# Optimization experiments

Measured on AMD Instinct MI355X. Metric: run time of the kernel, lower is better.

The kernel has to match this reference:

```python
import jax, jax.numpy as jnp
import numpy as np

C = 1024
MID = C // 4  # 256
B, H, W = 16, 56, 56


def setup_inputs() -> dict:
    key = jax.random.key(0)
    ks = jax.random.split(key, 8)
    x = jax.random.normal(ks[0], (B, C, H, W), dtype=jnp.float32)
    gate_values = jax.random.uniform(ks[1], (B, MID), dtype=jnp.float32)
    # MoELayer conv weights: stack of out_channels 1x1 convs -> [out, in]
    W1 = jax.random.normal(ks[2], (MID, C), dtype=jnp.float32) * (1.0 / np.sqrt(C))
    b1 = jnp.zeros((MID,), dtype=jnp.float32)
    W2 = jax.random.normal(ks[3], (MID, MID), dtype=jnp.float32) * (1.0 / np.sqrt(MID))
    b2 = jnp.zeros((MID,), dtype=jnp.float32)
    W3 = jax.random.normal(ks[4], (C, MID), dtype=jnp.float32) * (1.0 / np.sqrt(MID))
    b3 = jnp.zeros((C,), dtype=jnp.float32)
    return {"x": x, "gate_values": gate_values, "W1": W1, "b1": b1,
            "W2": W2, "b2": b2, "W3": W3, "b3": b3}


def _moe_1x1(h, gate, Wc, bc):
    # Dense equivalent of the per-channel gated 1x1 conv experts:
    # out[b,o] = (conv_o(h[b]) ) * gate[b,o] if gate[b,o] > 0 else 0
    y = jnp.einsum('bchw,oc->bohw', h, Wc) + bc[None, :, None, None]
    g = jnp.where(gate > 0, gate, 0.0)  # [B, O]
    return y * g[:, :, None, None]


def reference(x, gate_values, W1, b1, W2, b2, W3, b3):
    h = jax.nn.relu(_moe_1x1(x, gate_values, W1, b1))
    h = jax.nn.relu(_moe_1x1(h, gate_values, W2, b2))
    h = jax.nn.relu(jnp.einsum('bchw,oc->bohw', h, W3) + b3[None, :, None, None])
    return h + x
```

## Files before the change

### kernel.cpp

```cpp
#include <hip/hip_runtime.h>


#define NPIX 3136
#define BATCH 16

typedef __attribute__((ext_vector_type(8))) short short8;
typedef __attribute__((ext_vector_type(4))) float v4f;

__device__ __forceinline__ unsigned short f2bf(float f) {
    union { float f; unsigned u; } v; v.f = f;
    unsigned r = v.u + 0x7fffu + ((v.u >> 16) & 1u);
    return (unsigned short)(r >> 16);
}

__device__ __forceinline__ void ld_g2l16(const unsigned short* g, unsigned short* l) {
    __builtin_amdgcn_global_load_lds(
        (const __attribute__((address_space(1))) unsigned int*)g,
        (__attribute__((address_space(3))) unsigned int*)l,
        16, 0, 0);
}

__device__ __forceinline__ void stage_w(const unsigned short* wg, int rowstride,
                                        unsigned short* wr, int t) {
    ld_g2l16(wg,                  wr + t * 8);
    ld_g2l16(wg + 64 * rowstride, wr + 2048 + t * 8);
    ld_g2l16(wg + 128 * rowstride, wr + 4096 + t * 8);
    ld_g2l16(wg + 192 * rowstride, wr + 6144 + t * 8);
}

__device__ __forceinline__ void bar_lds_only() {
    asm volatile("s_waitcnt lgkmcnt(0)" ::: "memory");
    __builtin_amdgcn_s_barrier();
    __builtin_amdgcn_sched_barrier(0);
}

__global__ void convert_w(const float* __restrict__ W1, const float* __restrict__ W2,
                          const float* __restrict__ W3, unsigned short* __restrict__ Wb) {
    size_t e = ((size_t)blockIdx.x * 256 + threadIdx.x) * 4;
    const float* src; size_t off;
    if (e < 262144)      { src = W1; off = e; }
    else if (e < 327680) { src = W2; off = e - 262144; }
    else                 { src = W3; off = e - 327680; }
    float4 v = *reinterpret_cast<const float4*>(&src[off]);
    uint2 p;
    p.x = (unsigned)f2bf(v.x) | ((unsigned)f2bf(v.y) << 16);
    p.y = (unsigned)f2bf(v.z) | ((unsigned)f2bf(v.w) << 16);
    *reinterpret_cast<uint2*>(&Wb[e]) = p;
}

__global__ __launch_bounds__(256, 2) void moe_block(
    const float* __restrict__ x, const unsigned short* __restrict__ Wb,
    const float* __restrict__ b1, const float* __restrict__ b2,
    const float* __restrict__ b3, const float* __restrict__ gate,
    float* __restrict__ out)
{
    __shared__ __attribute__((aligned(16))) unsigned short Wsm[2 * 8192];
    __shared__ __attribute__((aligned(16))) unsigned short Hsm[64 * 256];
    __shared__ __attribute__((aligned(16))) unsigned short Xsm[64 * 32];

    const unsigned short* W1b = Wb;
    const unsigned short* W2b = Wb + 262144;
    const unsigned short* W3b = Wb + 327680;

    const int b    = blockIdx.z;
    const int p0   = blockIdx.x * 64;
    const int t    = threadIdx.x;
    const int lane = t & 63;
    const int wave = t >> 6;
    const int wm   = wave * 64;
    const int l15  = lane & 15;
    const int quad = lane >> 4;

    const int srow  = t >> 2;
    const int skoff = (t & 3) * 8;

    char* hb = reinterpret_cast<char*>(Hsm);
    v4f acc[4][4];

    const unsigned short* wg1 = W1b + srow * 1024 + skoff;
    const unsigned short* wg2 = W2b + srow * 256 + skoff;
    const unsigned short* wg3 = W3b + srow * 256 + skoff;

    #pragma unroll
    for (int i = 0; i < 4; ++i)
        #pragma unroll
        for (int j = 0; j < 4; ++j) acc[i][j] = (v4f){0.f, 0.f, 0.f, 0.f};

    {
        const int cp   = t & 15;
        const int pgrp = t >> 4;
        const float* xg = x + ((size_t)(b * 1024 + 2 * cp)) * NPIX + p0 + pgrp * 4;
        unsigned* xw = reinterpret_cast<unsigned*>(&Xsm[pgrp * 128 + 2 * cp]);

        stage_w(wg1, 1024, Wsm, t);
        float4 a0 = *reinterpret_cast<const float4*>(xg);
        float4 a1 = *reinterpret_cast<const float4*>(xg + NPIX);
        __syncthreads();

        for (int kt = 0; kt < 32; ++kt) {
            unsigned short* rd = Wsm + (kt & 1) * 8192;
            unsigned short* wr = Wsm + ((kt & 1) ^ 1) * 8192;

            unsigned u0 = (unsigned)f2bf(a0.x) | ((unsigned)f2bf(a1.x) << 16);
            unsigned u1 = (unsigned)f2bf(a0.y) | ((unsigned)f2bf(a1.y) << 16);
            unsigned u2 = (unsigned)f2bf(a0.z) | ((unsigned)f2bf(a1.z) << 16);
            unsigned u3 = (unsigned)f2bf(a0.w) | ((unsigned)f2bf(a1.w) << 16);
            xw[0] = u0; xw[16] = u1; xw[32] = u2; xw[48] = u3;

            if (kt < 31) stage_w(wg1 + (kt + 1) * 32, 1024, wr, t);
            else         stage_w(wg2, 256, wr, t);
            if (kt < 31) {
                const float* xp = xg + (size_t)(kt + 1) * 32 * NPIX;
                a0 = *reinterpret_cast<const float4*>(xp);
                a1 = *reinterpret_cast<const float4*>(xp + NPIX);
            }

            bar_lds_only();

            short8 rf[4], cf[4];
            #pragma unroll
            for (int mt = 0; mt < 4; ++mt)
                rf[mt] = *reinterpret_cast<const short8*>(
                    &rd[(wm + mt * 16 + l15) * 32 + quad * 8]);
            #pragma unroll
            for (int nt = 0; nt < 4; ++nt)
                cf[nt] = *reinterpret_cast<const short8*>(
                    &Xsm[(nt * 16 + l15) * 32 + quad * 8]);
            #pragma unroll
            for (int mt = 0; mt < 4; ++mt)
                #pragma unroll
                for (int nt = 0; nt < 4; ++nt)
                    acc[mt][nt] = __builtin_amdgcn_mfma_f32_16x16x32_bf16(
                        rf[mt], cf[nt], acc[mt][nt], 0, 0, 0);

            __syncthreads();
        }
    }

    #pragma unroll
    for (int mt = 0; mt < 4; ++mt) {
        const int o = wm + mt * 16 + quad * 4;
        const float4 bi = *reinterpret_cast<const float4*>(&b1[o]);
        const float4 gv = *reinterpret_cast<const float4*>(&gate[b * 256 + o]);
        const float g0 = gv.x > 0.f ? gv.x : 0.f;
        const float g1 = gv.y > 0.f ? gv.y : 0.f;
        const float g2 = gv.z > 0.f ? gv.z : 0.f;
        const float g3 = gv.w > 0.f ? gv.w : 0.f;
        #pragma unroll
        for (int nt = 0; nt < 4; ++nt) {
            const int pix = nt * 16 + l15;
            float v0 = (acc[mt][nt][0] + bi.x) * g0;
            float v1 = (acc[mt][nt][1] + bi.y) * g1;
            float v2 = (acc[mt][nt][2] + bi.z) * g2;
            float v3 = (acc[mt][nt][3] + bi.w) * g3;
            v0 = v0 > 0.f ? v0 : 0.f; v1 = v1 > 0.f ? v1 : 0.f;
            v2 = v2 > 0.f ? v2 : 0.f; v3 = v3 > 0.f ? v3 : 0.f;
            uint2 pq;
            pq.x = (unsigned)f2bf(v0) | ((unsigned)f2bf(v1) << 16);
            pq.y = (unsigned)f2bf(v2) | ((unsigned)f2bf(v3) << 16);
            const unsigned off = (unsigned)(pix * 512 + o * 2) ^ (unsigned)((pix & 7) << 4);
            *reinterpret_cast<uint2*>(hb + off) = pq;
        }
    }
    __syncthreads();

    #pragma unroll
    for (int i = 0; i < 4; ++i)
        #pragma unroll
        for (int j = 0; j < 4; ++j) acc[i][j] = (v4f){0.f, 0.f, 0.f, 0.f};

    for (int bt = 0; bt < 8; ++bt) {
        unsigned short* rd = Wsm + (bt & 1) * 8192;
        unsigned short* wr = Wsm + ((bt & 1) ^ 1) * 8192;
        if (bt < 7) stage_w(wg2 + (bt + 1) * 32, 256, wr, t);
        else        stage_w(wg3, 256, wr, t);

        const int k0 = bt * 32;
        short8 rf[4], cf[4];
        #pragma unroll
        for (int mt = 0; mt < 4; ++mt)
            rf[mt] = *reinterpret_cast<const short8*>(
                &rd[(wm + mt * 16 + l15) * 32 + quad * 8]);
        #pragma unroll
        for (int nt = 0; nt < 4; ++nt) {
            const int row = nt * 16 + l15;
            const unsigned off =
                (unsigned)(row * 512 + k0 * 2 + quad * 16) ^ (unsigned)((row & 7) << 4);
            cf[nt] = *reinterpret_cast<const short8*>(hb + off);
        }
        #pragma unroll
        for (int mt = 0; mt < 4; ++mt)
            #pragma unroll
            for (int nt = 0; nt < 4; ++nt)
                acc[mt][nt] = __builtin_amdgcn_mfma_f32_16x16x32_bf16(
                    rf[mt], cf[nt], acc[mt][nt], 0, 0, 0);

        __syncthreads();
    }

    #pragma unroll
    for (int mt = 0; mt < 4; ++mt) {
        const int o = wm + mt * 16 + quad * 4;
        const float4 bi = *reinterpret_cast<const float4*>(&b2[o]);
        const float4 gv = *reinterpret_cast<const float4*>(&gate[b * 256 + o]);
        const float g0 = gv.x > 0.f ? gv.x : 0.f;
        const float g1 = gv.y > 0.f ? gv.y : 0.f;
        const float g2 = gv.z > 0.f ? gv.z : 0.f;
        const float g3 = gv.w > 0.f ? gv.w : 0.f;
        #pragma unroll
        for (int nt = 0; nt < 4; ++nt) {
            const int pix = nt * 16 + l15;
            float v0 = (acc[mt][nt][0] + bi.x) * g0;
            float v1 = (acc[mt][nt][1] + bi.y) * g1;
            float v2 = (acc[mt][nt][2] + bi.z) * g2;
            float v3 = (acc[mt][nt][3] + bi.w) * g3;
            v0 = v0 > 0.f ? v0 : 0.f; v1 = v1 > 0.f ? v1 : 0.f;
            v2 = v2 > 0.f ? v2 : 0.f; v3 = v3 > 0.f ? v3 : 0.f;
            uint2 pq;
            pq.x = (unsigned)f2bf(v0) | ((unsigned)f2bf(v1) << 16);
            pq.y = (unsigned)f2bf(v2) | ((unsigned)f2bf(v3) << 16);
            const unsigned off = (unsigned)(pix * 512 + o * 2) ^ (unsigned)((pix & 7) << 4);
            *reinterpret_cast<uint2*>(hb + off) = pq;
        }
    }
    __syncthreads();

    #pragma unroll
    for (int i = 0; i < 4; ++i)
        #pragma unroll
        for (int j = 0; j < 4; ++j) acc[i][j] = (v4f){0.f, 0.f, 0.f, 0.f};

    for (int jt = 0; jt < 32; ++jt) {
        unsigned short* rd = Wsm + (jt & 1) * 8192;
        unsigned short* wr = Wsm + ((jt & 1) ^ 1) * 8192;
        if (jt < 31) {
            const int jn = jt + 1;
            stage_w(wg3 + (jn >> 3) * 65536 + (jn & 7) * 32, 256, wr, t);
        }

        const int k0 = (jt & 7) * 32;
        short8 rf[4], cf[4];
        #pragma unroll
        for (int mt = 0; mt < 4; ++mt) {
            const int row = mt * 16 + l15;
            const unsigned off =
                (unsigned)(row * 512 + k0 * 2 + quad * 16) ^ (unsigned)((row & 7) << 4);
            rf[mt] = *reinterpret_cast<const short8*>(hb + off);
        }
        #pragma unroll
        for (int nt = 0; nt < 4; ++nt)
            cf[nt] = *reinterpret_cast<const short8*>(
                &rd[(wm + nt * 16 + l15) * 32 + quad * 8]);
        #pragma unroll
        for (int mt = 0; mt < 4; ++mt)
            #pragma unroll
            for (int nt = 0; nt < 4; ++nt)
                acc[mt][nt] = __builtin_amdgcn_mfma_f32_16x16x32_bf16(
                    rf[mt], cf[nt], acc[mt][nt], 0, 0, 0);

        __syncthreads();

        if ((jt & 7) == 7) {
            const int oc0 = (jt >> 3) * 256;
            #pragma unroll
            for (int nt = 0; nt < 4; ++nt) {
                const int o = oc0 + wm + nt * 16 + l15;
                const float bi = b3[o];
                #pragma unroll
                for (int mt = 0; mt < 4; ++mt) {
                    const int pix = p0 + mt * 16 + quad * 4;
                    const size_t base = ((size_t)(b * 1024 + o)) * NPIX + pix;
                    const float4 xr = *reinterpret_cast<const float4*>(&x[base]);
                    float v0 = acc[mt][nt][0] + bi, v1 = acc[mt][nt][1] + bi;
                    float v2 = acc[mt][nt][2] + bi, v3 = acc[mt][nt][3] + bi;
                    float4 ov;
                    ov.x = (v0 > 0.f ? v0 : 0.f) + xr.x;
                    ov.y = (v1 > 0.f ? v1 : 0.f) + xr.y;
                    ov.z = (v2 > 0.f ? v2 : 0.f) + xr.z;
                    ov.w = (v3 > 0.f ? v3 : 0.f) + xr.w;
                    *reinterpret_cast<float4*>(&out[base]) = ov;
                }
            }
            #pragma unroll
            for (int i = 0; i < 4; ++i)
                #pragma unroll
                for (int j = 0; j < 4; ++j) acc[i][j] = (v4f){0.f, 0.f, 0.f, 0.f};
        }
    }
}

extern "C" void kernel_launch(void* const* d_in, const int* in_sizes, int n_in,
                              void* d_out, int out_size, void* d_ws, size_t ws_size,
                              hipStream_t stream) {
    const float* x    = (const float*)d_in[0];
    const float* gate = (const float*)d_in[1];
    const float* W1   = (const float*)d_in[2];
    const float* b1   = (const float*)d_in[3];
    const float* W2   = (const float*)d_in[4];
    const float* b2   = (const float*)d_in[5];
    const float* W3   = (const float*)d_in[6];
    const float* b3   = (const float*)d_in[7];
    float* out = (float*)d_out;

    unsigned short* Wb = (unsigned short*)d_ws;

    dim3 blk(256);
    convert_w<<<576, blk, 0, stream>>>(W1, W2, W3, Wb);
    moe_block<<<dim3(49, 1, BATCH), blk, 0, stream>>>(x, Wb, b1, b2, b3, gate, out);
}
```

Measured before the change: 502.8 us.

## Load weight fragments directly from global, drop LDS weight staging, raise occupancy

Removes the double-buffered LDS staging of weight tiles. Each wave now reads its bf16 weight MFMA fragments straight from global memory (L2-resident) into registers, and only the activation tile is double-buffered in LDS. This removes most block-wide barriers in all three GEMM stages and shrinks LDS use, so launch bounds rise from 2 to 4 blocks per CU. The cost is uncoalesced, redundant global or cache reads of the weights, whose latency is no longer hidden behind a prefetch stage, plus extra register pressure from the higher occupancy target.

```diff
diff --git a/kernel.cpp b/kernel.cpp
--- a/kernel.cpp
+++ b/kernel.cpp
@@ -13,19 +13,8 @@
     return (unsigned short)(r >> 16);
 }
 
-__device__ __forceinline__ void ld_g2l16(const unsigned short* g, unsigned short* l) {
-    __builtin_amdgcn_global_load_lds(
-        (const __attribute__((address_space(1))) unsigned int*)g,
-        (__attribute__((address_space(3))) unsigned int*)l,
-        16, 0, 0);
-}
-
-__device__ __forceinline__ void stage_w(const unsigned short* wg, int rowstride,
-                                        unsigned short* wr, int t) {
-    ld_g2l16(wg,                  wr + t * 8);
-    ld_g2l16(wg + 64 * rowstride, wr + 2048 + t * 8);
-    ld_g2l16(wg + 128 * rowstride, wr + 4096 + t * 8);
-    ld_g2l16(wg + 192 * rowstride, wr + 6144 + t * 8);
+__device__ __forceinline__ short8 ldg8(const unsigned short* p) {
+    return *reinterpret_cast<const short8*>(p);
 }
 
 __device__ __forceinline__ void bar_lds_only() {
@@ -48,15 +37,14 @@
     *reinterpret_cast<uint2*>(&Wb[e]) = p;
 }
 
-__global__ __launch_bounds__(256, 2) void moe_block(
+__global__ __launch_bounds__(256, 4) void moe_block(
     const float* __restrict__ x, const unsigned short* __restrict__ Wb,
     const float* __restrict__ b1, const float* __restrict__ b2,
     const float* __restrict__ b3, const float* __restrict__ gate,
     float* __restrict__ out)
 {
-    __shared__ __attribute__((aligned(16))) unsigned short Wsm[2 * 8192];
     __shared__ __attribute__((aligned(16))) unsigned short Hsm[64 * 256];
-    __shared__ __attribute__((aligned(16))) unsigned short Xsm[64 * 32];
+    __shared__ __attribute__((aligned(16))) unsigned short Xsm[2][64 * 32];
 
     const unsigned short* W1b = Wb;
     const unsigned short* W2b = Wb + 262144;
@@ -71,15 +59,12 @@
     const int l15  = lane & 15;
     const int quad = lane >> 4;
 
-    const int srow  = t >> 2;
-    const int skoff = (t & 3) * 8;
-
     char* hb = reinterpret_cast<char*>(Hsm);
     v4f acc[4][4];
 
-    const unsigned short* wg1 = W1b + srow * 1024 + skoff;
-    const unsigned short* wg2 = W2b + srow * 256 + skoff;
-    const unsigned short* wg3 = W3b + srow * 256 + skoff;
+    const unsigned short* wf1 = W1b + (size_t)(wm + l15) * 1024 + quad * 8;
+    const unsigned short* wf2 = W2b + (size_t)(wm + l15) * 256 + quad * 8;
+    const unsigned short* wf3 = W3b + (size_t)(wm + l15) * 256 + quad * 8;
 
     #pragma unroll
     for (int i = 0; i < 4; ++i)
@@ -90,50 +75,49 @@
         const int cp   = t & 15;
         const int pgrp = t >> 4;
         const float* xg = x + ((size_t)(b * 1024 + 2 * cp)) * NPIX + p0 + pgrp * 4;
-        unsigned* xw = reinterpret_cast<unsigned*>(&Xsm[pgrp * 128 + 2 * cp]);
-
-        stage_w(wg1, 1024, Wsm, t);
+
         float4 a0 = *reinterpret_cast<const float4*>(xg);
         float4 a1 = *reinterpret_cast<const float4*>(xg + NPIX);
-        __syncthreads();
-
-        for (int kt = 0; kt < 32; ++kt) {
-            unsigned short* rd = Wsm + (kt & 1) * 8192;
-            unsigned short* wr = Wsm + ((kt & 1) ^ 1) * 8192;
-
+        {
+            unsigned* xw = reinterpret_cast<unsigned*>(&Xsm[0][pgrp * 128 + 2 * cp]);
             unsigned u0 = (unsigned)f2bf(a0.x) | ((unsigned)f2bf(a1.x) << 16);
             unsigned u1 = (unsigned)f2bf(a0.y) | ((unsigned)f2bf(a1.y) << 16);
             unsigned u2 = (unsigned)f2bf(a0.z) | ((unsigned)f2bf(a1.z) << 16);
             unsigned u3 = (unsigned)f2bf(a0.w) | ((unsigned)f2bf(a1.w) << 16);
             xw[0] = u0; xw[16] = u1; xw[32] = u2; xw[48] = u3;
-
-            if (kt < 31) stage_w(wg1 + (kt + 1) * 32, 1024, wr, t);
-            else         stage_w(wg2, 256, wr, t);
+        }
+        bar_lds_only();
+
+        for (int kt = 0; kt < 32; ++kt) {
             if (kt < 31) {
                 const float* xp = xg + (size_t)(kt + 1) * 32 * NPIX;
                 a0 = *reinterpret_cast<const float4*>(xp);
                 a1 = *reinterpret_cast<const float4*>(xp + NPIX);
             }
-
-            bar_lds_only();
-
             short8 rf[4], cf[4];
             #pragma unroll
             for (int mt = 0; mt < 4; ++mt)
-                rf[mt] = *reinterpret_cast<const short8*>(
-                    &rd[(wm + mt * 16 + l15) * 32 + quad * 8]);
+                rf[mt] = ldg8(wf1 + (size_t)mt * 16384 + kt * 32);
             #pragma unroll
             for (int nt = 0; nt < 4; ++nt)
                 cf[nt] = *reinterpret_cast<const short8*>(
-                    &Xsm[(nt * 16 + l15) * 32 + quad * 8]);
+                    &Xsm[kt & 1][(nt * 16 + l15) * 32 + quad * 8]);
             #pragma unroll
             for (int mt = 0; mt < 4; ++mt)
                 #pragma unroll
                 for (int nt = 0; nt < 4; ++nt)
                     acc[mt][nt] = __builtin_amdgcn_mfma_f32_16x16x32_bf16(
                         rf[mt], cf[nt], acc[mt][nt], 0, 0, 0);
-
-            __syncthreads();
+            if (kt < 31) {
+                unsigned* xw = reinterpret_cast<unsigned*>(
+                    &Xsm[(kt + 1) & 1][pgrp * 128 + 2 * cp]);
+                unsigned u0 = (unsigned)f2bf(a0.x) | ((unsigned)f2bf(a1.x) << 16);
+                unsigned u1 = (unsigned)f2bf(a0.y) | ((unsigned)f2bf(a1.y) << 16);
+                unsigned u2 = (unsigned)f2bf(a0.z) | ((unsigned)f2bf(a1.z) << 16);
+                unsigned u3 = (unsigned)f2bf(a0.w) | ((unsigned)f2bf(a1.w) << 16);
+                xw[0] = u0; xw[16] = u1; xw[32] = u2; xw[48] = u3;
+                bar_lds_only();
+            }
         }
     }
 
@@ -169,23 +153,17 @@
         #pragma unroll
         for (int j = 0; j < 4; ++j) acc[i][j] = (v4f){0.f, 0.f, 0.f, 0.f};
 
+    #pragma unroll
     for (int bt = 0; bt < 8; ++bt) {
-        unsigned short* rd = Wsm + (bt & 1) * 8192;
-        unsigned short* wr = Wsm + ((bt & 1) ^ 1) * 8192;
-        if (bt < 7) stage_w(wg2 + (bt + 1) * 32, 256, wr, t);
-        else        stage_w(wg3, 256, wr, t);
-
-        const int k0 = bt * 32;
         short8 rf[4], cf[4];
         #pragma unroll
         for (int mt = 0; mt < 4; ++mt)
-            rf[mt] = *reinterpret_cast<const short8*>(
-                &rd[(wm + mt * 16 + l15) * 32 + quad * 8]);
+            rf[mt] = ldg8(wf2 + (size_t)mt * 4096 + bt * 32);
         #pragma unroll
         for (int nt = 0; nt < 4; ++nt) {
             const int row = nt * 16 + l15;
             const unsigned off =
-                (unsigned)(row * 512 + k0 * 2 + quad * 16) ^ (unsigned)((row & 7) << 4);
+                (unsigned)(row * 512 + bt * 64 + quad * 16) ^ (unsigned)((row & 7) << 4);
             cf[nt] = *reinterpret_cast<const short8*>(hb + off);
         }
         #pragma unroll
@@ -194,9 +172,8 @@
             for (int nt = 0; nt < 4; ++nt)
                 acc[mt][nt] = __builtin_amdgcn_mfma_f32_16x16x32_bf16(
                     rf[mt], cf[nt], acc[mt][nt], 0, 0, 0);
-
-        __syncthreads();
-    }
+    }
+    __syncthreads();
 
     #pragma unroll
     for (int mt = 0; mt < 4; ++mt) {
@@ -225,66 +202,53 @@
     }
     __syncthreads();
 
-    #pragma unroll
-    for (int i = 0; i < 4; ++i)
-        #pragma unroll
-        for (int j = 0; j < 4; ++j) acc[i][j] = (v4f){0.f, 0.f, 0.f, 0.f};
-
-    for (int jt = 0; jt < 32; ++jt) {
-        unsigned short* rd = Wsm + (jt & 1) * 8192;
-        unsigned short* wr = Wsm + ((jt & 1) ^ 1) * 8192;
-        if (jt < 31) {
-            const int jn = jt + 1;
-            stage_w(wg3 + (jn >> 3) * 65536 + (jn & 7) * 32, 256, wr, t);
-        }
-
-        const int k0 = (jt & 7) * 32;
-        short8 rf[4], cf[4];
-        #pragma unroll
-        for (int mt = 0; mt < 4; ++mt) {
-            const int row = mt * 16 + l15;
-            const unsigned off =
-                (unsigned)(row * 512 + k0 * 2 + quad * 16) ^ (unsigned)((row & 7) << 4);
-            rf[mt] = *reinterpret_cast<const short8*>(hb + off);
-        }
-        #pragma unroll
-        for (int nt = 0; nt < 4; ++nt)
-            cf[nt] = *reinterpret_cast<const short8*>(
-                &rd[(wm + nt * 16 + l15) * 32 + quad * 8]);
-        #pragma unroll
-        for (int mt = 0; mt < 4; ++mt)
+    for (int ch = 0; ch < 4; ++ch) {
+        const int oc0 = ch * 256;
+        #pragma unroll
+        for (int i = 0; i < 4; ++i)
+            #pragma unroll
+            for (int j = 0; j < 4; ++j) acc[i][j] = (v4f){0.f, 0.f, 0.f, 0.f};
+
+        #pragma unroll
+        for (int jt = 0; jt < 8; ++jt) {
+            const int k0 = jt * 32;
+            short8 rf[4], cf[4];
+            #pragma unroll
+            for (int mt = 0; mt < 4; ++mt) {
+                const int row = mt * 16 + l15;
+                const unsigned off =
+                    (unsigned)(row * 512 + k0 * 2 + quad * 16) ^ (unsigned)((row & 7) << 4);
+                rf[mt] = *reinterpret_cast<const short8*>(hb + off);
+            }
             #pragma unroll
             for (int nt = 0; nt < 4; ++nt)
-                acc[mt][nt] = __builtin_amdgcn_mfma_f32_16x16x32_bf16(
-                    rf[mt], cf[nt], acc[mt][nt], 0, 0, 0);
-
-        __syncthreads();
-
-        if ((jt & 7) == 7) {
-            const int oc0 = (jt >> 3) * 256;
-            #pragma unroll
-            for (int nt = 0; nt < 4; ++nt) {
-                const int o = oc0 + wm + nt * 16 + l15;
-                const float bi = b3[o];
+                cf[nt] = ldg8(wf3 + (size_t)(oc0 + nt * 16) * 256 + k0);
+            #pragma unroll
+            for (int mt = 0; mt < 4; ++mt)
                 #pragma unroll
-                for (int mt = 0; mt < 4; ++mt) {
-                    const int pix = p0 + mt * 16 + quad * 4;
-                    const size_t base = ((size_t)(b * 1024 + o)) * NPIX + pix;
-                    const float4 xr = *reinterpret_cast<const float4*>(&x[base]);
-                    float v0 = acc[mt][nt][0] + bi, v1 = acc[mt][nt][1] + bi;
-                    float v2 = acc[mt][nt][2] + bi, v3 = acc[mt][nt][3] + bi;
-                    float4 ov;
-                    ov.x = (v0 > 0.f ? v0 : 0.f) + xr.x;
-                    ov.y = (v1 > 0.f ? v1 : 0.f) + xr.y;
-                    ov.z = (v2 > 0.f ? v2 : 0.f) + xr.z;
-                    ov.w = (v3 > 0.f ? v3 : 0.f) + xr.w;
-                    *reinterpret_cast<float4*>(&out[base]) = ov;
-                }
-            }
-            #pragma unroll
-            for (int i = 0; i < 4; ++i)
-                #pragma unroll
-                for (int j = 0; j < 4; ++j) acc[i][j] = (v4f){0.f, 0.f, 0.f, 0.f};
+                for (int nt = 0; nt < 4; ++nt)
+                    acc[mt][nt] = __builtin_amdgcn_mfma_f32_16x16x32_bf16(
+                        rf[mt], cf[nt], acc[mt][nt], 0, 0, 0);
+        }
+
+        #pragma unroll
+        for (int nt = 0; nt < 4; ++nt) {
+            const int o = oc0 + wm + nt * 16 + l15;
+            const float bi = b3[o];
+            #pragma unroll
+            for (int mt = 0; mt < 4; ++mt) {
+                const int pix = p0 + mt * 16 + quad * 4;
+                const size_t base = ((size_t)(b * 1024 + o)) * NPIX + pix;
+                const float4 xr = *reinterpret_cast<const float4*>(&x[base]);
+                float v0 = acc[mt][nt][0] + bi, v1 = acc[mt][nt][1] + bi;
+                float v2 = acc[mt][nt][2] + bi, v3 = acc[mt][nt][3] + bi;
+                float4 ov;
+                ov.x = (v0 > 0.f ? v0 : 0.f) + xr.x;
+                ov.y = (v1 > 0.f ? v1 : 0.f) + xr.y;
+                ov.z = (v2 > 0.f ? v2 : 0.f) + xr.z;
+                ov.w = (v3 > 0.f ? v3 : 0.f) + xr.w;
+                *reinterpret_cast<float4*>(&out[base]) = ov;
+            }
         }
     }
 }
```

New measurement: 641.4 us. 1.28x slower.
